# Performance work log

Hardware: AMD Instinct MI355X
Metric: run time of the kernel (lower is better)

## Reference

```python
import jax, jax.numpy as jnp
import numpy as np

BETA = 0.1       # reputation weight
GAMMA = 0.1      # load penalty weight
EXPL_C = 0.1     # UCB exploration constant
LOAD_EMA = 0.9   # load EMA alpha
TOP_K = 2
EPS = 1e-10


def setup_inputs() -> dict:
    key = jax.random.key(0)
    k1, k2, k3, k4, k5 = jax.random.split(key, 5)
    B, S, H, E = 4, 4096, 2048, 64
    return {
        "x": jax.random.normal(k1, (B, S, H), dtype=jnp.float32),
        "gate_w": jax.random.normal(k2, (E, H), dtype=jnp.float32) * (1.0 / np.sqrt(H)),
        "reputation": jax.random.normal(k3, (E,), dtype=jnp.float32),
        "loads": jax.random.uniform(k4, (E,), dtype=jnp.float32),
        "counts": jax.random.uniform(k5, (E,), dtype=jnp.float32),
        "total_decisions": 1000000,
    }


def reference(x, gate_w, reputation, loads, counts, total_decisions):
    B, S, H = x.shape
    E = gate_w.shape[0]
    x_flat = x.reshape(-1, H)                                  # [T, H]
    base_logits = jnp.einsum("th,eh->te", x_flat, gate_w)      # [T, E]

    # current_batch_assignments is None -> current_loads = expert_loads
    updated_loads = LOAD_EMA * loads + (1.0 - LOAD_EMA) * loads  # [E]

    # UCB-style exploration bonus, broadcast over tokens
    expl = EXPL_C * jnp.sqrt(jnp.log(jnp.float32(total_decisions) + 1.0) / (counts + EPS))  # [E]

    selection_scores = (base_logits
                        + BETA * reputation[None, :]
                        - GAMMA * updated_loads[None, :]
                        + expl[None, :])                        # [T, E]

    top_k_scores, top_k_indices = jax.lax.top_k(selection_scores, TOP_K)  # [T, K]
    routing_weights = jax.nn.softmax(top_k_scores, axis=-1).reshape(B, S, TOP_K)
    expert_indices = top_k_indices.reshape(B, S, TOP_K)

    # differentiable load-balancing aux loss
    router_probs = jax.nn.softmax(selection_scores.astype(jnp.float32), axis=-1)  # [T, E]
    expert_gate = jax.nn.one_hot(top_k_indices, E, dtype=jnp.float32).sum(axis=1)  # [T, E]
    tokens_per_expert = expert_gate.mean(axis=0)               # [E]
    router_prob_per_expert = router_probs.mean(axis=0)         # [E]
    aux_loss = (tokens_per_expert * router_prob_per_expert).sum() * E

    return routing_weights, expert_indices, aux_loss
```

## Files before the change

### kernel.cpp

```cpp
#include <hip/hip_runtime.h>
#include <hip/hip_bf16.h>
#include <cmath>

#define HDIM 2048
#define H4   (HDIM / 4)
#define NEXP 64
#define TTOT 16384
#define KSPLIT 2
#define KBLK (HDIM / KSPLIT)
#define BKC  64
#define NCHUNK (KBLK / BKC)
#define BTOK 64
#define LDT  72
#define LDS_SC 65

typedef unsigned short u16;
typedef short  bf16x8 __attribute__((ext_vector_type(8)));
typedef float  f32x16 __attribute__((ext_vector_type(16)));

#define WS_GWS_OFF   128
#define GWS_FLOATS   (3 * NEXP * HDIM / 2)
#define WS_PARTIAL_OFF (WS_GWS_OFF + GWS_FLOATS)
#define PARTIAL_FLOATS ((size_t)(TTOT / BTOK) * KSPLIT * BTOK * NEXP)
#define ESTR (NEXP * HDIM)

__device__ __forceinline__ unsigned cvtpk(float a, float b) {
    __hip_bfloat162 h2 = __float22bfloat162_rn(make_float2(a, b));
    unsigned r;
    __builtin_memcpy(&r, &h2, sizeof(r));
    return r;
}
__device__ __forceinline__ void split3(float4 f, uint2* H, uint2* M, uint2* L) {
    unsigned h0 = cvtpk(f.x, f.y), h1 = cvtpk(f.z, f.w);
    float r0 = f.x - __uint_as_float(h0 << 16);
    float r1 = f.y - __uint_as_float(h0 & 0xffff0000u);
    float r2 = f.z - __uint_as_float(h1 << 16);
    float r3 = f.w - __uint_as_float(h1 & 0xffff0000u);
    unsigned m0 = cvtpk(r0, r1), m1 = cvtpk(r2, r3);
    float s0 = r0 - __uint_as_float(m0 << 16);
    float s1 = r1 - __uint_as_float(m0 & 0xffff0000u);
    float s2 = r2 - __uint_as_float(m1 << 16);
    float s3 = r3 - __uint_as_float(m1 & 0xffff0000u);
    unsigned l0 = cvtpk(s0, s1), l1 = cvtpk(s2, s3);
    *H = make_uint2(h0, h1); *M = make_uint2(m0, m1); *L = make_uint2(l0, l1);
}

__global__ __launch_bounds__(256) void split_gw_k(
    const float* __restrict__ gw, u16* __restrict__ gws,
    float* __restrict__ accs)
{
    const int i = blockIdx.x * 256 + threadIdx.x;
    if (blockIdx.x == 0 && threadIdx.x < 2 * NEXP) accs[threadIdx.x] = 0.0f;
    float4 f = reinterpret_cast<const float4*>(gw)[i];
    uint2 h, m, l;
    split3(f, &h, &m, &l);
    reinterpret_cast<uint2*>(gws)[i]            = h;
    reinterpret_cast<uint2*>(gws + ESTR)[i]     = m;
    reinterpret_cast<uint2*>(gws + 2 * ESTR)[i] = l;
}

__global__ __launch_bounds__(256, 2) void router_gemm_mfma(
    const float* __restrict__ x,
    const u16*   __restrict__ gws,
    float* __restrict__ partial)
{
    __shared__ short aT[3][BTOK][LDT];
    __shared__ short bT[3][NEXP][LDT];

    const int tid  = threadIdx.x;
    const int lane = tid & 63;
    const int l31  = lane & 31;
    const int lhi  = lane >> 5;
    const int w    = tid >> 6;
    const int wm   = w & 1;
    const int wn   = w >> 1;
    const int tb   = blockIdx.x;
    const int kg   = blockIdx.y;
    const int T0   = tb * BTOK;

    const int srow = tid >> 2;
    const int scol = tid & 3;

    const float4* __restrict__ x4 = reinterpret_cast<const float4*>(x)
        + (size_t)(T0 + srow) * H4 + (size_t)kg * (H4 / 2) + scol;
    const u16* __restrict__ gwsB = gws + (size_t)srow * HDIM + kg * KBLK + scol * 16;

    f32x16 acc;
    #pragma unroll
    for (int i = 0; i < 16; ++i) acc[i] = 0.0f;

    const short* aP[3];
    const short* bP[3];
    #pragma unroll
    for (int v = 0; v < 3; ++v) {
        aP[v] = &aT[v][32 * wm + l31][8 * lhi];
        bP[v] = &bT[v][32 * wn + l31][8 * lhi];
    }

    float4 xa[4];

#define LOAD_CHUNK(CH) do {                                                    \
        _Pragma("unroll")                                                      \
        for (int j = 0; j < 4; ++j)                                            \
            xa[j] = x4[(CH) * (BKC / 4) + 4 * j];                              \
    } while (0)

    LOAD_CHUNK(0);

    for (int ch = 0; ch < NCHUNK; ++ch) {
        uint4 bq[3][2];
        #pragma unroll
        for (int v = 0; v < 3; ++v) {
            const u16* p = gwsB + (size_t)v * ESTR + ch * 64;
            bq[v][0] = *reinterpret_cast<const uint4*>(p);
            bq[v][1] = *reinterpret_cast<const uint4*>(p + 8);
        }
        #pragma unroll
        for (int j = 0; j < 4; ++j) {
            uint2 h, m, l;
            split3(xa[j], &h, &m, &l);
            const int kl = 4 * (scol + 4 * j);
            *reinterpret_cast<uint2*>(&aT[0][srow][kl]) = h;
            *reinterpret_cast<uint2*>(&aT[1][srow][kl]) = m;
            *reinterpret_cast<uint2*>(&aT[2][srow][kl]) = l;
        }
        #pragma unroll
        for (int v = 0; v < 3; ++v) {
            *reinterpret_cast<uint4*>(&bT[v][srow][scol * 16])     = bq[v][0];
            *reinterpret_cast<uint4*>(&bT[v][srow][scol * 16 + 8]) = bq[v][1];
        }
        __syncthreads();

        if (ch + 1 < NCHUNK) LOAD_CHUNK(ch + 1);

        #pragma unroll
        for (int ks = 0; ks < 4; ++ks) {
            bf16x8 ah = *reinterpret_cast<const bf16x8*>(aP[0] + 16 * ks);
            bf16x8 am = *reinterpret_cast<const bf16x8*>(aP[1] + 16 * ks);
            bf16x8 al = *reinterpret_cast<const bf16x8*>(aP[2] + 16 * ks);
            bf16x8 bh = *reinterpret_cast<const bf16x8*>(bP[0] + 16 * ks);
            bf16x8 bm = *reinterpret_cast<const bf16x8*>(bP[1] + 16 * ks);
            bf16x8 bl = *reinterpret_cast<const bf16x8*>(bP[2] + 16 * ks);
            acc = __builtin_amdgcn_mfma_f32_32x32x16_bf16(ah, bh, acc, 0, 0, 0);
            acc = __builtin_amdgcn_mfma_f32_32x32x16_bf16(ah, bm, acc, 0, 0, 0);
            acc = __builtin_amdgcn_mfma_f32_32x32x16_bf16(am, bh, acc, 0, 0, 0);
            acc = __builtin_amdgcn_mfma_f32_32x32x16_bf16(ah, bl, acc, 0, 0, 0);
            acc = __builtin_amdgcn_mfma_f32_32x32x16_bf16(am, bm, acc, 0, 0, 0);
            acc = __builtin_amdgcn_mfma_f32_32x32x16_bf16(al, bh, acc, 0, 0, 0);
        }
        __syncthreads();
    }
#undef LOAD_CHUNK

    float* pbase = partial + ((size_t)tb * KSPLIT + kg) * (BTOK * NEXP);
    const int e = 32 * wn + l31;
    #pragma unroll
    for (int r = 0; r < 16; ++r) {
        const int t_loc = 32 * wm + (r & 3) + 8 * (r >> 2) + 4 * lhi;
        pbase[(size_t)t_loc * NEXP + e] = acc[r];
    }
}

__global__ __launch_bounds__(256) void router_reduce(
    const float* __restrict__ partial,
    const float* __restrict__ rep,
    const float* __restrict__ loads,
    const float* __restrict__ counts,
    const int*   __restrict__ total_dec,
    float* __restrict__ out_w,
    float* __restrict__ out_idx,
    float* __restrict__ prob_acc,
    float* __restrict__ gate_acc)
{
    __shared__ float sc_s[BTOK][LDS_SC];
    __shared__ float bias_s[NEXP];
    __shared__ float m_s[BTOK], zi_s[BTOK];
    __shared__ int   i1_s[BTOK], i2_s[BTOK];

    const int tid = threadIdx.x;
    const int rt  = blockIdx.x;
    const int t0  = rt * BTOK;

    if (tid < NEXP) {
        float L = logf((float)(*total_dec) + 1.0f);
        bias_s[tid] = 0.1f * rep[tid] - 0.1f * loads[tid]
                    + 0.1f * sqrtf(L / (counts[tid] + 1e-10f));
    }
    __syncthreads();

    const float* p = partial + (size_t)rt * KSPLIT * (BTOK * NEXP);
    #pragma unroll
    for (int o = 0; o < (BTOK * NEXP) / 256; ++o) {
        const int idx = o * 256 + tid;
        float s = p[idx] + p[BTOK * NEXP + idx];
        sc_s[idx >> 6][idx & 63] = s + bias_s[idx & 63];
    }
    __syncthreads();

    if (tid < BTOK) {
        const int t = tid;
        float m1 = -INFINITY, m2 = -INFINITY;
        int   i1 = 0, i2 = 0;
        for (int e = 0; e < NEXP; ++e) {
            const float s = sc_s[t][e];
            if (s > m1)      { m2 = m1; i2 = i1; m1 = s; i1 = e; }
            else if (s > m2) { m2 = s; i2 = e; }
        }
        float z = 0.0f;
        for (int e = 0; e < NEXP; ++e) z += __expf(sc_s[t][e] - m1);

        const float e2  = expf(m2 - m1);
        const float inv = 1.0f / (1.0f + e2);
        const int   gt  = t0 + t;
        reinterpret_cast<float2*>(out_w)[gt]   = make_float2(inv, e2 * inv);
        reinterpret_cast<float2*>(out_idx)[gt] = make_float2((float)i1, (float)i2);
        m_s[t] = m1; zi_s[t] = 1.0f / z; i1_s[t] = i1; i2_s[t] = i2;
    }
    __syncthreads();

    if (tid < NEXP) {
        const int e = tid;
        float ps = 0.0f, gs = 0.0f;
        for (int t = 0; t < BTOK; ++t) {
            ps += __expf(sc_s[t][e] - m_s[t]) * zi_s[t];
            gs += (float)((i1_s[t] == e) + (i2_s[t] == e));
        }
        atomicAdd(&prob_acc[e], ps);
        atomicAdd(&gate_acc[e], gs);
    }
}

#define BKF  32
#define LDAF (64 + 4)
__global__ __launch_bounds__(256) void router_main(
    const float* __restrict__ x,
    const float* __restrict__ gw,
    const float* __restrict__ rep,
    const float* __restrict__ loads,
    const float* __restrict__ counts,
    const int*   __restrict__ total_dec,
    float* __restrict__ out_w,
    float* __restrict__ out_idx,
    float* __restrict__ prob_acc,
    float* __restrict__ gate_acc)
{
    __shared__ float a_s[2][BKF][LDAF];
    __shared__ float b_s[2][BKF][LDAF];
    __shared__ float sc_s[64][LDS_SC];
    __shared__ float bias_s[NEXP];
    __shared__ float m_s[64], z_s[64];
    __shared__ int   i1_s[64], i2_s[64];

    const int tid = threadIdx.x;
    const int tx  = tid & 15;
    const int ty  = tid >> 4;
    const int r0  = tid >> 3;
    const int c4  = tid & 7;
    const int t0  = blockIdx.x * 64;

    if (tid < NEXP) {
        float L = logf((float)(*total_dec) + 1.0f);
        bias_s[tid] = 0.1f * rep[tid] - 0.1f * loads[tid]
                    + 0.1f * sqrtf(L / (counts[tid] + 1e-10f));
    }

    const float4* __restrict__ x4 = reinterpret_cast<const float4*>(x) + (size_t)t0 * H4;
    const float4* __restrict__ g4 = reinterpret_cast<const float4*>(gw);

    float acc[4][4] = {};

#define STORE_TILE(BUFI, A0, A1, B0, B1) do {                                  \
        float _t0[4] = {(A0).x, (A0).y, (A0).z, (A0).w};                       \
        float _t1[4] = {(A1).x, (A1).y, (A1).z, (A1).w};                       \
        float _t2[4] = {(B0).x, (B0).y, (B0).z, (B0).w};                       \
        float _t3[4] = {(B1).x, (B1).y, (B1).z, (B1).w};                       \
        _Pragma("unroll")                                                      \
        for (int u = 0; u < 4; ++u) {                                          \
            a_s[BUFI][c4 * 4 + u][r0]      = _t0[u];                           \
            a_s[BUFI][c4 * 4 + u][r0 + 32] = _t1[u];                           \
            b_s[BUFI][c4 * 4 + u][r0]      = _t2[u];                           \
            b_s[BUFI][c4 * 4 + u][r0 + 32] = _t3[u];                           \
        } } while (0)

    {
        float4 a0 = x4[(size_t)r0 * H4 + c4];
        float4 a1 = x4[(size_t)(r0 + 32) * H4 + c4];
        float4 b0 = g4[(size_t)r0 * H4 + c4];
        float4 b1 = g4[(size_t)(r0 + 32) * H4 + c4];
        STORE_TILE(0, a0, a1, b0, b1);
    }
    __syncthreads();

    int buf = 0;
    for (int it = 0; it < HDIM / BKF; ++it) {
        float4 na0, na1, nb0, nb1;
        const bool has_next = (it + 1 < HDIM / BKF);
        if (has_next) {
            const int k4 = (it + 1) * (BKF / 4);
            na0 = x4[(size_t)r0 * H4 + k4 + c4];
            na1 = x4[(size_t)(r0 + 32) * H4 + k4 + c4];
            nb0 = g4[(size_t)r0 * H4 + k4 + c4];
            nb1 = g4[(size_t)(r0 + 32) * H4 + k4 + c4];
        }
        #pragma unroll
        for (int kk = 0; kk < BKF; ++kk) {
            const float4 afv = *reinterpret_cast<const float4*>(&a_s[buf][kk][ty * 4]);
            const float4 bfv = *reinterpret_cast<const float4*>(&b_s[buf][kk][tx * 4]);
            const float af[4] = {afv.x, afv.y, afv.z, afv.w};
            const float bf[4] = {bfv.x, bfv.y, bfv.z, bfv.w};
            #pragma unroll
            for (int i = 0; i < 4; ++i)
                #pragma unroll
                for (int j = 0; j < 4; ++j)
                    acc[i][j] = fmaf(af[i], bf[j], acc[i][j]);
        }
        if (has_next) STORE_TILE(buf ^ 1, na0, na1, nb0, nb1);
        __syncthreads();
        buf ^= 1;
    }
#undef STORE_TILE

    #pragma unroll
    for (int i = 0; i < 4; ++i)
        #pragma unroll
        for (int j = 0; j < 4; ++j)
            sc_s[ty * 4 + i][tx * 4 + j] = acc[i][j] + bias_s[tx * 4 + j];
    __syncthreads();

    if (tid < 64) {
        const int t = tid;
        float m1 = -INFINITY, m2 = -INFINITY;
        int   i1 = 0, i2 = 0;
        for (int e = 0; e < NEXP; ++e) {
            const float s = sc_s[t][e];
            if (s > m1)      { m2 = m1; i2 = i1; m1 = s; i1 = e; }
            else if (s > m2) { m2 = s; i2 = e; }
        }
        float z = 0.0f;
        for (int e = 0; e < NEXP; ++e) z += expf(sc_s[t][e] - m1);
        const float e2  = expf(m2 - m1);
        const float inv = 1.0f / (1.0f + e2);
        const int   gt  = t0 + t;
        reinterpret_cast<float2*>(out_w)[gt]   = make_float2(inv, e2 * inv);
        reinterpret_cast<float2*>(out_idx)[gt] = make_float2((float)i1, (float)i2);
        m_s[t] = m1; z_s[t] = z; i1_s[t] = i1; i2_s[t] = i2;
    }
    __syncthreads();

    if (tid < NEXP) {
        const int e = tid;
        float ps = 0.0f, gs = 0.0f;
        for (int t = 0; t < 64; ++t) {
            ps += expf(sc_s[t][e] - m_s[t]) / z_s[t];
            gs += (float)((i1_s[t] == e) + (i2_s[t] == e));
        }
        atomicAdd(&prob_acc[e], ps);
        atomicAdd(&gate_acc[e], gs);
    }
}

__global__ void router_aux(const float* __restrict__ prob_acc,
                           const float* __restrict__ gate_acc,
                           float* __restrict__ out_aux)
{
    const float invT = 1.0f / (float)TTOT;
    const int e = threadIdx.x;
    float v = (gate_acc[e] * invT) * (prob_acc[e] * invT);
    #pragma unroll
    for (int off = 32; off > 0; off >>= 1)
        v += __shfl_down(v, off);
    if (e == 0) out_aux[0] = v * (float)NEXP;
}

extern "C" void kernel_launch(void* const* d_in, const int* in_sizes, int n_in,
                              void* d_out, int out_size, void* d_ws, size_t ws_size,
                              hipStream_t stream)
{
    const float* x      = (const float*)d_in[0];
    const float* gw     = (const float*)d_in[1];
    const float* rep    = (const float*)d_in[2];
    const float* loads  = (const float*)d_in[3];
    const float* counts = (const float*)d_in[4];
    const int*   total  = (const int*)d_in[5];

    float* out     = (float*)d_out;
    float* out_w   = out;
    float* out_idx = out + 32768;
    float* out_aux = out + 65536;

    float* prob_acc = (float*)d_ws;
    float* gate_acc = prob_acc + NEXP;
    u16*   gws      = (u16*)((float*)d_ws + WS_GWS_OFF);
    float* partial  = (float*)d_ws + WS_PARTIAL_OFF;

    const size_t ws_needed = (WS_PARTIAL_OFF + PARTIAL_FLOATS) * sizeof(float);

    if (ws_size >= ws_needed) {
        split_gw_k<<<dim3(NEXP * HDIM / 4 / 256), dim3(256), 0, stream>>>(
            gw, gws, prob_acc);
        router_gemm_mfma<<<dim3(TTOT / BTOK, KSPLIT), dim3(256), 0, stream>>>(
            x, gws, partial);
        router_reduce<<<dim3(TTOT / BTOK), dim3(256), 0, stream>>>(
            partial, rep, loads, counts, total, out_w, out_idx, prob_acc, gate_acc);
    } else {
        (void)hipMemsetAsync(d_ws, 0, 2 * NEXP * sizeof(float), stream);
        router_main<<<dim3(TTOT / 64), dim3(256), 0, stream>>>(
            x, gw, rep, loads, counts, total, out_w, out_idx, prob_acc, gate_acc);
    }
    router_aux<<<dim3(1), dim3(64), 0, stream>>>(prob_acc, gate_acc, out_aux);
}
```

Measured before the change: 231.9 us.

## Fuse gate-split, MFMA GEMM and top-k reduce into one kernel with intra-block K-split

After: 294.7 us. +27.1%, slower.

```diff
diff --git a/kernel.cpp b/kernel.cpp
--- a/kernel.cpp
+++ b/kernel.cpp
@@ -6,11 +6,10 @@
 #define H4   (HDIM / 4)
 #define NEXP 64
 #define TTOT 16384
-#define KSPLIT 2
-#define KBLK (HDIM / KSPLIT)
 #define BKC  64
-#define NCHUNK (KBLK / BKC)
+#define NCHUNK (HDIM / BKC)
 #define BTOK 64
+#define NBLK (TTOT / BTOK)
 #define LDT  72
 #define LDS_SC 65
 
@@ -18,11 +17,7 @@
 typedef short  bf16x8 __attribute__((ext_vector_type(8)));
 typedef float  f32x16 __attribute__((ext_vector_type(16)));
 
-#define WS_GWS_OFF   128
-#define GWS_FLOATS   (3 * NEXP * HDIM / 2)
-#define WS_PARTIAL_OFF (WS_GWS_OFF + GWS_FLOATS)
-#define PARTIAL_FLOATS ((size_t)(TTOT / BTOK) * KSPLIT * BTOK * NEXP)
-#define ESTR (NEXP * HDIM)
+#define WS_FLOATS (2 * NBLK * NEXP)
 
 __device__ __forceinline__ unsigned cvtpk(float a, float b) {
     __hip_bfloat162 h2 = __float22bfloat162_rn(make_float2(a, b));
@@ -45,27 +40,26 @@
     *H = make_uint2(h0, h1); *M = make_uint2(m0, m1); *L = make_uint2(l0, l1);
 }
 
-__global__ __launch_bounds__(256) void split_gw_k(
-    const float* __restrict__ gw, u16* __restrict__ gws,
-    float* __restrict__ accs)
+__global__ __launch_bounds__(512) void router_fused(
+    const float* __restrict__ x,
+    const float* __restrict__ gw,
+    const float* __restrict__ rep,
+    const float* __restrict__ loads,
+    const float* __restrict__ counts,
+    const int*   __restrict__ total_dec,
+    float* __restrict__ out_w,
+    float* __restrict__ out_idx,
+    float* __restrict__ prob_part,
+    float* __restrict__ gate_part)
 {
-    const int i = blockIdx.x * 256 + threadIdx.x;
-    if (blockIdx.x == 0 && threadIdx.x < 2 * NEXP) accs[threadIdx.x] = 0.0f;
-    float4 f = reinterpret_cast<const float4*>(gw)[i];
-    uint2 h, m, l;
-    split3(f, &h, &m, &l);
-    reinterpret_cast<uint2*>(gws)[i]            = h;
-    reinterpret_cast<uint2*>(gws + ESTR)[i]     = m;
-    reinterpret_cast<uint2*>(gws + 2 * ESTR)[i] = l;
-}
-
-__global__ __launch_bounds__(256, 2) void router_gemm_mfma(
-    const float* __restrict__ x,
-    const u16*   __restrict__ gws,
-    float* __restrict__ partial)
-{
-    __shared__ short aT[3][BTOK][LDT];
-    __shared__ short bT[3][NEXP][LDT];
+    __shared__ __align__(16) char pool[2 * 3 * BTOK * LDT * sizeof(short)];
+    short (*aT)[BTOK][LDT] = reinterpret_cast<short (*)[BTOK][LDT]>(pool);
+    short (*bT)[BTOK][LDT] =
+        reinterpret_cast<short (*)[BTOK][LDT]>(pool + 3 * BTOK * LDT * sizeof(short));
+    float (*sc_s)[LDS_SC] = reinterpret_cast<float (*)[LDS_SC]>(pool);
+    __shared__ float bias_s[NEXP];
+    __shared__ float m_s[BTOK], zi_s[BTOK];
+    __shared__ int   i1_s[BTOK], i2_s[BTOK];
 
     const int tid  = threadIdx.x;
     const int lane = tid & 63;
@@ -73,17 +67,24 @@
     const int lhi  = lane >> 5;
     const int w    = tid >> 6;
     const int wm   = w & 1;
-    const int wn   = w >> 1;
-    const int tb   = blockIdx.x;
-    const int kg   = blockIdx.y;
-    const int T0   = tb * BTOK;
-
-    const int srow = tid >> 2;
-    const int scol = tid & 3;
+    const int wn   = (w >> 1) & 1;
+    const int kh   = w >> 2;
+    const int rt   = blockIdx.x;
+    const int T0   = rt * BTOK;
+
+    if (tid < NEXP) {
+        float L = logf((float)(*total_dec) + 1.0f);
+        bias_s[tid] = 0.1f * rep[tid] - 0.1f * loads[tid]
+                    + 0.1f * sqrtf(L / (counts[tid] + 1e-10f));
+    }
+
+    const int srow = tid >> 3;
+    const int scol = tid & 7;
 
     const float4* __restrict__ x4 = reinterpret_cast<const float4*>(x)
-        + (size_t)(T0 + srow) * H4 + (size_t)kg * (H4 / 2) + scol;
-    const u16* __restrict__ gwsB = gws + (size_t)srow * HDIM + kg * KBLK + scol * 16;
+        + (size_t)(T0 + srow) * H4 + scol * 2;
+    const float4* __restrict__ g4 = reinterpret_cast<const float4*>(gw)
+        + (size_t)srow * H4 + scol * 2;
 
     f32x16 acc;
     #pragma unroll
@@ -97,50 +98,45 @@
         bP[v] = &bT[v][32 * wn + l31][8 * lhi];
     }
 
-    float4 xa[4];
-
-#define LOAD_CHUNK(CH) do {                                                    \
-        _Pragma("unroll")                                                      \
-        for (int j = 0; j < 4; ++j)                                            \
-            xa[j] = x4[(CH) * (BKC / 4) + 4 * j];                              \
+    float4 xa[2][2], xg[2][2];
+
+#define LOAD_CHUNK(CH, SLOT) do {                                              \
+        xa[SLOT][0] = x4[(CH) * 16];  xa[SLOT][1] = x4[(CH) * 16 + 1];         \
+        xg[SLOT][0] = g4[(CH) * 16];  xg[SLOT][1] = g4[(CH) * 16 + 1];         \
     } while (0)
 
-    LOAD_CHUNK(0);
+#define SPLIT_STORE8(TILE, F0, F1) do {                                        \
+        uint2 h0, m0, l0, h1, m1, l1;                                          \
+        split3(F0, &h0, &m0, &l0);                                             \
+        split3(F1, &h1, &m1, &l1);                                             \
+        const int kl = scol * 8;                                               \
+        *reinterpret_cast<uint4*>(&TILE[0][srow][kl]) =                        \
+            make_uint4(h0.x, h0.y, h1.x, h1.y);                                \
+        *reinterpret_cast<uint4*>(&TILE[1][srow][kl]) =                        \
+            make_uint4(m0.x, m0.y, m1.x, m1.y);                                \
+        *reinterpret_cast<uint4*>(&TILE[2][srow][kl]) =                        \
+            make_uint4(l0.x, l0.y, l1.x, l1.y);                                \
+    } while (0)
+
+    LOAD_CHUNK(0, 0);
+    LOAD_CHUNK(1, 1);
 
     for (int ch = 0; ch < NCHUNK; ++ch) {
-        uint4 bq[3][2];
-        #pragma unroll
-        for (int v = 0; v < 3; ++v) {
-            const u16* p = gwsB + (size_t)v * ESTR + ch * 64;
-            bq[v][0] = *reinterpret_cast<const uint4*>(p);
-            bq[v][1] = *reinterpret_cast<const uint4*>(p + 8);
-        }
-        #pragma unroll
-        for (int j = 0; j < 4; ++j) {
-            uint2 h, m, l;
-            split3(xa[j], &h, &m, &l);
-            const int kl = 4 * (scol + 4 * j);
-            *reinterpret_cast<uint2*>(&aT[0][srow][kl]) = h;
-            *reinterpret_cast<uint2*>(&aT[1][srow][kl]) = m;
-            *reinterpret_cast<uint2*>(&aT[2][srow][kl]) = l;
-        }
-        #pragma unroll
-        for (int v = 0; v < 3; ++v) {
-            *reinterpret_cast<uint4*>(&bT[v][srow][scol * 16])     = bq[v][0];
-            *reinterpret_cast<uint4*>(&bT[v][srow][scol * 16 + 8]) = bq[v][1];
-        }
+        const int slot = ch & 1;
+        SPLIT_STORE8(aT, xa[slot][0], xa[slot][1]);
+        SPLIT_STORE8(bT, xg[slot][0], xg[slot][1]);
+        if (ch + 2 < NCHUNK) LOAD_CHUNK(ch + 2, slot);
         __syncthreads();
 
-        if (ch + 1 < NCHUNK) LOAD_CHUNK(ch + 1);
-
-        #pragma unroll
-        for (int ks = 0; ks < 4; ++ks) {
-            bf16x8 ah = *reinterpret_cast<const bf16x8*>(aP[0] + 16 * ks);
-            bf16x8 am = *reinterpret_cast<const bf16x8*>(aP[1] + 16 * ks);
-            bf16x8 al = *reinterpret_cast<const bf16x8*>(aP[2] + 16 * ks);
-            bf16x8 bh = *reinterpret_cast<const bf16x8*>(bP[0] + 16 * ks);
-            bf16x8 bm = *reinterpret_cast<const bf16x8*>(bP[1] + 16 * ks);
-            bf16x8 bl = *reinterpret_cast<const bf16x8*>(bP[2] + 16 * ks);
+        #pragma unroll
+        for (int s = 0; s < 2; ++s) {
+            const int ko = 16 * (2 * kh + s);
+            bf16x8 ah = *reinterpret_cast<const bf16x8*>(aP[0] + ko);
+            bf16x8 am = *reinterpret_cast<const bf16x8*>(aP[1] + ko);
+            bf16x8 al = *reinterpret_cast<const bf16x8*>(aP[2] + ko);
+            bf16x8 bh = *reinterpret_cast<const bf16x8*>(bP[0] + ko);
+            bf16x8 bm = *reinterpret_cast<const bf16x8*>(bP[1] + ko);
+            bf16x8 bl = *reinterpret_cast<const bf16x8*>(bP[2] + ko);
             acc = __builtin_amdgcn_mfma_f32_32x32x16_bf16(ah, bh, acc, 0, 0, 0);
             acc = __builtin_amdgcn_mfma_f32_32x32x16_bf16(ah, bm, acc, 0, 0, 0);
             acc = __builtin_amdgcn_mfma_f32_32x32x16_bf16(am, bh, acc, 0, 0, 0);
@@ -151,49 +147,23 @@
         __syncthreads();
     }
 #undef LOAD_CHUNK
-
-    float* pbase = partial + ((size_t)tb * KSPLIT + kg) * (BTOK * NEXP);
+#undef SPLIT_STORE8
+
     const int e = 32 * wn + l31;
-    #pragma unroll
-    for (int r = 0; r < 16; ++r) {
-        const int t_loc = 32 * wm + (r & 3) + 8 * (r >> 2) + 4 * lhi;
-        pbase[(size_t)t_loc * NEXP + e] = acc[r];
-    }
-}
-
-__global__ __launch_bounds__(256) void router_reduce(
-    const float* __restrict__ partial,
-    const float* __restrict__ rep,
-    const float* __restrict__ loads,
-    const float* __restrict__ counts,
-    const int*   __restrict__ total_dec,
-    float* __restrict__ out_w,
-    float* __restrict__ out_idx,
-    float* __restrict__ prob_acc,
-    float* __restrict__ gate_acc)
-{
-    __shared__ float sc_s[BTOK][LDS_SC];
-    __shared__ float bias_s[NEXP];
-    __shared__ float m_s[BTOK], zi_s[BTOK];
-    __shared__ int   i1_s[BTOK], i2_s[BTOK];
-
-    const int tid = threadIdx.x;
-    const int rt  = blockIdx.x;
-    const int t0  = rt * BTOK;
-
-    if (tid < NEXP) {
-        float L = logf((float)(*total_dec) + 1.0f);
-        bias_s[tid] = 0.1f * rep[tid] - 0.1f * loads[tid]
-                    + 0.1f * sqrtf(L / (counts[tid] + 1e-10f));
-    }
-    __syncthreads();
-
-    const float* p = partial + (size_t)rt * KSPLIT * (BTOK * NEXP);
-    #pragma unroll
-    for (int o = 0; o < (BTOK * NEXP) / 256; ++o) {
-        const int idx = o * 256 + tid;
-        float s = p[idx] + p[BTOK * NEXP + idx];
-        sc_s[idx >> 6][idx & 63] = s + bias_s[idx & 63];
+    if (kh == 0) {
+        #pragma unroll
+        for (int r = 0; r < 16; ++r) {
+            const int t_loc = 32 * wm + (r & 3) + 8 * (r >> 2) + 4 * lhi;
+            sc_s[t_loc][e] = acc[r];
+        }
+    }
+    __syncthreads();
+    if (kh == 1) {
+        #pragma unroll
+        for (int r = 0; r < 16; ++r) {
+            const int t_loc = 32 * wm + (r & 3) + 8 * (r >> 2) + 4 * lhi;
+            sc_s[t_loc][e] += acc[r] + bias_s[e];
+        }
     }
     __syncthreads();
 
@@ -201,17 +171,17 @@
         const int t = tid;
         float m1 = -INFINITY, m2 = -INFINITY;
         int   i1 = 0, i2 = 0;
-        for (int e = 0; e < NEXP; ++e) {
-            const float s = sc_s[t][e];
-            if (s > m1)      { m2 = m1; i2 = i1; m1 = s; i1 = e; }
-            else if (s > m2) { m2 = s; i2 = e; }
+        for (int ee = 0; ee < NEXP; ++ee) {
+            const float s = sc_s[t][ee];
+            if (s > m1)      { m2 = m1; i2 = i1; m1 = s; i1 = ee; }
+            else if (s > m2) { m2 = s; i2 = ee; }
         }
         float z = 0.0f;
-        for (int e = 0; e < NEXP; ++e) z += __expf(sc_s[t][e] - m1);
+        for (int ee = 0; ee < NEXP; ++ee) z += __expf(sc_s[t][ee] - m1);
 
         const float e2  = expf(m2 - m1);
         const float inv = 1.0f / (1.0f + e2);
-        const int   gt  = t0 + t;
+        const int   gt  = T0 + t;
         reinterpret_cast<float2*>(out_w)[gt]   = make_float2(inv, e2 * inv);
         reinterpret_cast<float2*>(out_idx)[gt] = make_float2((float)i1, (float)i2);
         m_s[t] = m1; zi_s[t] = 1.0f / z; i1_s[t] = i1; i2_s[t] = i2;
@@ -219,14 +189,41 @@
     __syncthreads();
 
     if (tid < NEXP) {
-        const int e = tid;
+        const int ee = tid;
         float ps = 0.0f, gs = 0.0f;
         for (int t = 0; t < BTOK; ++t) {
-            ps += __expf(sc_s[t][e] - m_s[t]) * zi_s[t];
-            gs += (float)((i1_s[t] == e) + (i2_s[t] == e));
-        }
-        atomicAdd(&prob_acc[e], ps);
-        atomicAdd(&gate_acc[e], gs);
+            ps += __expf(sc_s[t][ee] - m_s[t]) * zi_s[t];
+            gs += (float)((i1_s[t] == ee) + (i2_s[t] == ee));
+        }
+        prob_part[rt * NEXP + ee] = ps;
+        gate_part[rt * NEXP + ee] = gs;
+    }
+}
+
+__global__ __launch_bounds__(256) void router_aux2(
+    const float* __restrict__ prob_part,
+    const float* __restrict__ gate_part,
+    float* __restrict__ out_aux)
+{
+    __shared__ float rp[4][NEXP], rg[4][NEXP];
+    const int e = threadIdx.x & 63;
+    const int q = threadIdx.x >> 6;
+    float sp = 0.0f, sg = 0.0f;
+    for (int b = q * (NBLK / 4); b < (q + 1) * (NBLK / 4); ++b) {
+        sp += prob_part[b * NEXP + e];
+        sg += gate_part[b * NEXP + e];
+    }
+    rp[q][e] = sp; rg[q][e] = sg;
+    __syncthreads();
+    if (threadIdx.x < NEXP) {
+        float pT = rp[0][e] + rp[1][e] + rp[2][e] + rp[3][e];
+        float gT = rg[0][e] + rg[1][e] + rg[2][e] + rg[3][e];
+        const float invT = 1.0f / (float)TTOT;
+        float v = (gT * invT) * (pT * invT);
+        #pragma unroll
+        for (int off = 32; off > 0; off >>= 1)
+            v += __shfl_down(v, off);
+        if (e == 0) out_aux[0] = v * (float)NEXP;
     }
 }
 
@@ -388,24 +385,18 @@
     float* out_idx = out + 32768;
     float* out_aux = out + 65536;
 
-    float* prob_acc = (float*)d_ws;
-    float* gate_acc = prob_acc + NEXP;
-    u16*   gws      = (u16*)((float*)d_ws + WS_GWS_OFF);
-    float* partial  = (float*)d_ws + WS_PARTIAL_OFF;
-
-    const size_t ws_needed = (WS_PARTIAL_OFF + PARTIAL_FLOATS) * sizeof(float);
-
-    if (ws_size >= ws_needed) {
-        split_gw_k<<<dim3(NEXP * HDIM / 4 / 256), dim3(256), 0, stream>>>(
-            gw, gws, prob_acc);
-        router_gemm_mfma<<<dim3(TTOT / BTOK, KSPLIT), dim3(256), 0, stream>>>(
-            x, gws, partial);
-        router_reduce<<<dim3(TTOT / BTOK), dim3(256), 0, stream>>>(
-            partial, rep, loads, counts, total, out_w, out_idx, prob_acc, gate_acc);
+    if (ws_size >= (size_t)WS_FLOATS * sizeof(float)) {
+        float* prob_part = (float*)d_ws;
+        float* gate_part = prob_part + NBLK * NEXP;
+        router_fused<<<dim3(NBLK), dim3(512), 0, stream>>>(
+            x, gw, rep, loads, counts, total, out_w, out_idx, prob_part, gate_part);
+        router_aux2<<<dim3(1), dim3(256), 0, stream>>>(prob_part, gate_part, out_aux);
     } else {
+        float* prob_acc = (float*)d_ws;
+        float* gate_acc = prob_acc + NEXP;
         (void)hipMemsetAsync(d_ws, 0, 2 * NEXP * sizeof(float), stream);
         router_main<<<dim3(TTOT / 64), dim3(256), 0, stream>>>(
             x, gw, rep, loads, counts, total, out_w, out_idx, prob_acc, gate_acc);
-    }
-    router_aux<<<dim3(1), dim3(64), 0, stream>>>(prob_acc, gate_acc, out_aux);
-}
+        router_aux<<<dim3(1), dim3(64), 0, stream>>>(prob_acc, gate_acc, out_aux);
+    }
+}
```

## Raise K-split to 4 with smaller chunks, double-buffered x loads, per-block aux partials

Applied to the files above, without the earlier changes.

Result: slower. 238.1 us (+2.7%).

```diff
diff --git a/kernel.cpp b/kernel.cpp
--- a/kernel.cpp
+++ b/kernel.cpp
@@ -6,22 +6,24 @@
 #define H4   (HDIM / 4)
 #define NEXP 64
 #define TTOT 16384
-#define KSPLIT 2
+#define KSPLIT 4
 #define KBLK (HDIM / KSPLIT)
-#define BKC  64
+#define BKC  32
 #define NCHUNK (KBLK / BKC)
 #define BTOK 64
-#define LDT  72
+#define NBLK (TTOT / BTOK)
+#define LDT  40
 #define LDS_SC 65
 
 typedef unsigned short u16;
 typedef short  bf16x8 __attribute__((ext_vector_type(8)));
 typedef float  f32x16 __attribute__((ext_vector_type(16)));
 
-#define WS_GWS_OFF   128
-#define GWS_FLOATS   (3 * NEXP * HDIM / 2)
+#define WS_AUX_FLOATS  (2 * NBLK * NEXP)
+#define WS_GWS_OFF     WS_AUX_FLOATS
+#define GWS_FLOATS     (3 * NEXP * HDIM / 2)
 #define WS_PARTIAL_OFF (WS_GWS_OFF + GWS_FLOATS)
-#define PARTIAL_FLOATS ((size_t)(TTOT / BTOK) * KSPLIT * BTOK * NEXP)
+#define PARTIAL_FLOATS ((size_t)NBLK * KSPLIT * BTOK * NEXP)
 #define ESTR (NEXP * HDIM)
 
 __device__ __forceinline__ unsigned cvtpk(float a, float b) {
@@ -46,11 +48,9 @@
 }
 
 __global__ __launch_bounds__(256) void split_gw_k(
-    const float* __restrict__ gw, u16* __restrict__ gws,
-    float* __restrict__ accs)
+    const float* __restrict__ gw, u16* __restrict__ gws)
 {
     const int i = blockIdx.x * 256 + threadIdx.x;
-    if (blockIdx.x == 0 && threadIdx.x < 2 * NEXP) accs[threadIdx.x] = 0.0f;
     float4 f = reinterpret_cast<const float4*>(gw)[i];
     uint2 h, m, l;
     split3(f, &h, &m, &l);
@@ -59,7 +59,7 @@
     reinterpret_cast<uint2*>(gws + 2 * ESTR)[i] = l;
 }
 
-__global__ __launch_bounds__(256, 2) void router_gemm_mfma(
+__global__ __launch_bounds__(256, 4) void router_gemm_mfma(
     const float* __restrict__ x,
     const u16*   __restrict__ gws,
     float* __restrict__ partial)
@@ -82,8 +82,9 @@
     const int scol = tid & 3;
 
     const float4* __restrict__ x4 = reinterpret_cast<const float4*>(x)
-        + (size_t)(T0 + srow) * H4 + (size_t)kg * (H4 / 2) + scol;
-    const u16* __restrict__ gwsB = gws + (size_t)srow * HDIM + kg * KBLK + scol * 16;
+        + (size_t)(T0 + srow) * H4 + (size_t)kg * (KBLK / 4) + scol * 2;
+    const u16* __restrict__ gwsB =
+        gws + (size_t)srow * HDIM + kg * KBLK + scol * 8;
 
     f32x16 acc;
     #pragma unroll
@@ -97,44 +98,42 @@
         bP[v] = &bT[v][32 * wn + l31][8 * lhi];
     }
 
-    float4 xa[4];
-
-#define LOAD_CHUNK(CH) do {                                                    \
-        _Pragma("unroll")                                                      \
-        for (int j = 0; j < 4; ++j)                                            \
-            xa[j] = x4[(CH) * (BKC / 4) + 4 * j];                              \
+    float4 xa[2][2];
+
+#define LOAD_CHUNK(CH, SLOT) do {                                              \
+        xa[SLOT][0] = x4[(CH) * (BKC / 4)];                                    \
+        xa[SLOT][1] = x4[(CH) * (BKC / 4) + 1];                                \
     } while (0)
 
-    LOAD_CHUNK(0);
+    LOAD_CHUNK(0, 0);
+    LOAD_CHUNK(1, 1);
 
     for (int ch = 0; ch < NCHUNK; ++ch) {
-        uint4 bq[3][2];
-        #pragma unroll
-        for (int v = 0; v < 3; ++v) {
-            const u16* p = gwsB + (size_t)v * ESTR + ch * 64;
-            bq[v][0] = *reinterpret_cast<const uint4*>(p);
-            bq[v][1] = *reinterpret_cast<const uint4*>(p + 8);
-        }
-        #pragma unroll
-        for (int j = 0; j < 4; ++j) {
-            uint2 h, m, l;
-            split3(xa[j], &h, &m, &l);
-            const int kl = 4 * (scol + 4 * j);
-            *reinterpret_cast<uint2*>(&aT[0][srow][kl]) = h;
-            *reinterpret_cast<uint2*>(&aT[1][srow][kl]) = m;
-            *reinterpret_cast<uint2*>(&aT[2][srow][kl]) = l;
-        }
-        #pragma unroll
-        for (int v = 0; v < 3; ++v) {
-            *reinterpret_cast<uint4*>(&bT[v][srow][scol * 16])     = bq[v][0];
-            *reinterpret_cast<uint4*>(&bT[v][srow][scol * 16 + 8]) = bq[v][1];
-        }
+        const int slot = ch & 1;
+        uint4 bq[3];
+        #pragma unroll
+        for (int v = 0; v < 3; ++v)
+            bq[v] = *reinterpret_cast<const uint4*>(gwsB + (size_t)v * ESTR + ch * BKC);
+        {
+            uint2 h0, m0, l0, h1, m1, l1;
+            split3(xa[slot][0], &h0, &m0, &l0);
+            split3(xa[slot][1], &h1, &m1, &l1);
+            const int kl = scol * 8;
+            *reinterpret_cast<uint4*>(&aT[0][srow][kl]) =
+                make_uint4(h0.x, h0.y, h1.x, h1.y);
+            *reinterpret_cast<uint4*>(&aT[1][srow][kl]) =
+                make_uint4(m0.x, m0.y, m1.x, m1.y);
+            *reinterpret_cast<uint4*>(&aT[2][srow][kl]) =
+                make_uint4(l0.x, l0.y, l1.x, l1.y);
+        }
+        #pragma unroll
+        for (int v = 0; v < 3; ++v)
+            *reinterpret_cast<uint4*>(&bT[v][srow][scol * 8]) = bq[v];
+        if (ch + 2 < NCHUNK) LOAD_CHUNK(ch + 2, slot);
         __syncthreads();
 
-        if (ch + 1 < NCHUNK) LOAD_CHUNK(ch + 1);
-
-        #pragma unroll
-        for (int ks = 0; ks < 4; ++ks) {
+        #pragma unroll
+        for (int ks = 0; ks < 2; ++ks) {
             bf16x8 ah = *reinterpret_cast<const bf16x8*>(aP[0] + 16 * ks);
             bf16x8 am = *reinterpret_cast<const bf16x8*>(aP[1] + 16 * ks);
             bf16x8 al = *reinterpret_cast<const bf16x8*>(aP[2] + 16 * ks);
@@ -169,8 +168,8 @@
     const int*   __restrict__ total_dec,
     float* __restrict__ out_w,
     float* __restrict__ out_idx,
-    float* __restrict__ prob_acc,
-    float* __restrict__ gate_acc)
+    float* __restrict__ prob_part,
+    float* __restrict__ gate_part)
 {
     __shared__ float sc_s[BTOK][LDS_SC];
     __shared__ float bias_s[NEXP];
@@ -188,11 +187,12 @@
     }
     __syncthreads();
 
-    const float* p = partial + (size_t)rt * KSPLIT * (BTOK * NEXP);
-    #pragma unroll
-    for (int o = 0; o < (BTOK * NEXP) / 256; ++o) {
+    const int S = BTOK * NEXP;
+    const float* p = partial + (size_t)rt * KSPLIT * S;
+    #pragma unroll
+    for (int o = 0; o < S / 256; ++o) {
         const int idx = o * 256 + tid;
-        float s = p[idx] + p[BTOK * NEXP + idx];
+        float s = (p[idx] + p[S + idx]) + (p[2 * S + idx] + p[3 * S + idx]);
         sc_s[idx >> 6][idx & 63] = s + bias_s[idx & 63];
     }
     __syncthreads();
@@ -225,8 +225,35 @@
             ps += __expf(sc_s[t][e] - m_s[t]) * zi_s[t];
             gs += (float)((i1_s[t] == e) + (i2_s[t] == e));
         }
-        atomicAdd(&prob_acc[e], ps);
-        atomicAdd(&gate_acc[e], gs);
+        prob_part[rt * NEXP + e] = ps;
+        gate_part[rt * NEXP + e] = gs;
+    }
+}
+
+__global__ __launch_bounds__(256) void router_aux2(
+    const float* __restrict__ prob_part,
+    const float* __restrict__ gate_part,
+    float* __restrict__ out_aux)
+{
+    __shared__ float rp[4][NEXP], rg[4][NEXP];
+    const int e = threadIdx.x & 63;
+    const int q = threadIdx.x >> 6;
+    float sp = 0.0f, sg = 0.0f;
+    for (int b = q * (NBLK / 4); b < (q + 1) * (NBLK / 4); ++b) {
+        sp += prob_part[b * NEXP + e];
+        sg += gate_part[b * NEXP + e];
+    }
+    rp[q][e] = sp; rg[q][e] = sg;
+    __syncthreads();
+    if (threadIdx.x < NEXP) {
+        float pT = rp[0][e] + rp[1][e] + rp[2][e] + rp[3][e];
+        float gT = rg[0][e] + rg[1][e] + rg[2][e] + rg[3][e];
+        const float invT = 1.0f / (float)TTOT;
+        float v = (gT * invT) * (pT * invT);
+        #pragma unroll
+        for (int off = 32; off > 0; off >>= 1)
+            v += __shfl_down(v, off);
+        if (e == 0) out_aux[0] = v * (float)NEXP;
     }
 }
 
@@ -388,24 +415,26 @@
     float* out_idx = out + 32768;
     float* out_aux = out + 65536;
 
-    float* prob_acc = (float*)d_ws;
-    float* gate_acc = prob_acc + NEXP;
-    u16*   gws      = (u16*)((float*)d_ws + WS_GWS_OFF);
-    float* partial  = (float*)d_ws + WS_PARTIAL_OFF;
-
     const size_t ws_needed = (WS_PARTIAL_OFF + PARTIAL_FLOATS) * sizeof(float);
 
     if (ws_size >= ws_needed) {
-        split_gw_k<<<dim3(NEXP * HDIM / 4 / 256), dim3(256), 0, stream>>>(
-            gw, gws, prob_acc);
-        router_gemm_mfma<<<dim3(TTOT / BTOK, KSPLIT), dim3(256), 0, stream>>>(
+        float* prob_part = (float*)d_ws;
+        float* gate_part = prob_part + NBLK * NEXP;
+        u16*   gws       = (u16*)((float*)d_ws + WS_GWS_OFF);
+        float* partial   = (float*)d_ws + WS_PARTIAL_OFF;
+
+        split_gw_k<<<dim3(NEXP * HDIM / 4 / 256), dim3(256), 0, stream>>>(gw, gws);
+        router_gemm_mfma<<<dim3(NBLK, KSPLIT), dim3(256), 0, stream>>>(
             x, gws, partial);
-        router_reduce<<<dim3(TTOT / BTOK), dim3(256), 0, stream>>>(
-            partial, rep, loads, counts, total, out_w, out_idx, prob_acc, gate_acc);
+        router_reduce<<<dim3(NBLK), dim3(256), 0, stream>>>(
+            partial, rep, loads, counts, total, out_w, out_idx, prob_part, gate_part);
+        router_aux2<<<dim3(1), dim3(256), 0, stream>>>(prob_part, gate_part, out_aux);
     } else {
+        float* prob_acc = (float*)d_ws;
+        float* gate_acc = prob_acc + NEXP;
         (void)hipMemsetAsync(d_ws, 0, 2 * NEXP * sizeof(float), stream);
         router_main<<<dim3(TTOT / 64), dim3(256), 0, stream>>>(
             x, gw, rep, loads, counts, total, out_w, out_idx, prob_acc, gate_acc);
-    }
-    router_aux<<<dim3(1), dim3(64), 0, stream>>>(prob_acc, gate_acc, out_aux);
-}
+        router_aux<<<dim3(1), dim3(64), 0, stream>>>(prob_acc, gate_acc, out_aux);
+    }
+}
```
